# Performance work log

Measured on AMD Instinct MI355X. Metric: run time of the kernel, lower is better.

## Reference

```python
import jax, jax.numpy as jnp
import numpy as np

VOCAB = 100000
EMBED = 128

def setup_inputs() -> dict:
    key = jax.random.key(0)
    k1, k2, k3 = jax.random.split(key, 3)
    x = jax.random.randint(k1, (4096, 200), 0, VOCAB, dtype=jnp.int64)
    # torch Linear(vocab, embed): weight [embed, vocab], bias [embed]
    W = jax.random.normal(k2, (EMBED, VOCAB), dtype=jnp.float32) * (1.0 / np.sqrt(VOCAB))
    b = jax.random.normal(k3, (EMBED,), dtype=jnp.float32) * 0.01
    return {"x": x, "W": W, "b": b}

def reference(x, W, b):
    # one_hot(x) @ W.T + b  ==  gather rows of W.T at x, then add bias.
    # Same math as the original scatter+Linear, expressed as a row-gather.
    y = jnp.take(W.T, x, axis=0)  # [B, T, EMBED]
    return y + b
```

## Files before the change

### kernel.cpp

```cpp
#include <hip/hip_runtime.h>


#define EMB 128
#define TOK_PER_BLK 64

typedef float fx4 __attribute__((ext_vector_type(4)));

__global__ void transpose_W_kernel(const float* __restrict__ W,
                                   float* __restrict__ Wt, int V) {
    __shared__ float lds[64 * 129];
    const int v0 = blockIdx.x * 64;
    const int t  = threadIdx.x;

    #pragma unroll 8
    for (int j = t; j < 128 * 64; j += 256) {
        const int e    = j >> 6;
        const int vloc = j & 63;
        const int v    = v0 + vloc;
        float val = 0.0f;
        if (v < V) val = W[(size_t)e * V + v];
        lds[vloc * 129 + e] = val;
    }
    __syncthreads();

    #pragma unroll 8
    for (int j = t; j < 64 * 128; j += 256) {
        const int vloc = j >> 7;
        const int e    = j & 127;
        const int v    = v0 + vloc;
        if (v < V) Wt[(size_t)v * EMB + e] = lds[vloc * 129 + e];
    }
}

__global__ void gather_rows_kernel(const int* __restrict__ idx,
                                   const float* __restrict__ Wt,
                                   const float* __restrict__ bias,
                                   float* __restrict__ out, int ntok) {
    __shared__ int rows[TOK_PER_BLK];
    const int t    = threadIdx.x;
    const int tok0 = blockIdx.x * TOK_PER_BLK;

    if (t < TOK_PER_BLK) {
        const int tok = tok0 + t;
        rows[t] = (tok < ntok) ? idx[tok] : 0;
    }
    __syncthreads();

    const int q = t & 31;
    const int g = t >> 5;
    const fx4 bq = ((const fx4*)bias)[q];

    fx4 v[8];
    #pragma unroll
    for (int p = 0; p < 8; ++p) {
        const int row = rows[g + p * 8];
        v[p] = ((const fx4*)(Wt + (size_t)row * EMB))[q];
    }

    #pragma unroll
    for (int p = 0; p < 8; ++p) {
        const int tok = tok0 + g + p * 8;
        if (tok < ntok) {
            fx4 r = v[p] + bq;
            __builtin_nontemporal_store(r, (fx4*)(out + (size_t)tok * EMB) + q);
        }
    }
}

__global__ void gather_direct_kernel(const int* __restrict__ idx,
                                     const float* __restrict__ W,
                                     const float* __restrict__ bias,
                                     float* __restrict__ out, int ntok, int V) {
    const long long total  = (long long)ntok * EMB;
    const long long stride = (long long)gridDim.x * blockDim.x;
    for (long long i = (long long)blockIdx.x * blockDim.x + threadIdx.x;
         i < total; i += stride) {
        const int token = (int)(i >> 7);
        const int e     = (int)(i & (EMB - 1));
        out[i] = W[(size_t)e * V + idx[token]] + bias[e];
    }
}

extern "C" void kernel_launch(void* const* d_in, const int* in_sizes, int n_in,
                              void* d_out, int out_size, void* d_ws, size_t ws_size,
                              hipStream_t stream) {
    const int*   x = (const int*)d_in[0];
    const float* W = (const float*)d_in[1];
    const float* b = (const float*)d_in[2];
    float* out = (float*)d_out;

    const int ntok = in_sizes[0];
    const int V    = in_sizes[1] / EMB;

    const size_t need = (size_t)V * EMB * sizeof(float);
    if (ws_size >= need) {
        float* Wt = (float*)d_ws;
        const int tblocks = (V + 63) / 64;
        transpose_W_kernel<<<tblocks, 256, 0, stream>>>(W, Wt, V);
        const int gblocks = (ntok + TOK_PER_BLK - 1) / TOK_PER_BLK;
        gather_rows_kernel<<<gblocks, 256, 0, stream>>>(x, Wt, b, out, ntok);
    } else {
        gather_direct_kernel<<<2048, 256, 0, stream>>>(x, W, b, out, ntok, V);
    }
}
```

Baseline: 516.5 us.

## Fold bias into transposed table and use persistent grid-stride gather

Adds the bias during the W transpose, so the gathered rows already include it and the gather kernel only copies. The gather becomes a persistent kernel of 2560 blocks looping over 64-token tiles, and each thread reads its own indices straight from global memory instead of staging them in LDS behind a barrier. The aim is to remove the bias load and add, the shared-memory sync, and per-block launch overhead. In exchange the transpose does extra bias reads, and the fixed grid size may fit the CU count less well.

```diff
diff --git a/kernel.cpp b/kernel.cpp
--- a/kernel.cpp
+++ b/kernel.cpp
@@ -2,12 +2,12 @@
 
 
 #define EMB 128
-#define TOK_PER_BLK 64
 
 typedef float fx4 __attribute__((ext_vector_type(4)));
 
-__global__ void transpose_W_kernel(const float* __restrict__ W,
-                                   float* __restrict__ Wt, int V) {
+__global__ void transpose_bias_kernel(const float* __restrict__ W,
+                                      const float* __restrict__ bias,
+                                      float* __restrict__ Wt, int V) {
     __shared__ float lds[64 * 129];
     const int v0 = blockIdx.x * 64;
     const int t  = threadIdx.x;
@@ -28,41 +28,46 @@
         const int vloc = j >> 7;
         const int e    = j & 127;
         const int v    = v0 + vloc;
-        if (v < V) Wt[(size_t)v * EMB + e] = lds[vloc * 129 + e];
+        if (v < V) Wt[(size_t)v * EMB + e] = lds[vloc * 129 + e] + bias[e];
     }
 }
 
 __global__ void gather_rows_kernel(const int* __restrict__ idx,
                                    const float* __restrict__ Wt,
-                                   const float* __restrict__ bias,
                                    float* __restrict__ out, int ntok) {
-    __shared__ int rows[TOK_PER_BLK];
-    const int t    = threadIdx.x;
-    const int tok0 = blockIdx.x * TOK_PER_BLK;
-
-    if (t < TOK_PER_BLK) {
-        const int tok = tok0 + t;
-        rows[t] = (tok < ntok) ? idx[tok] : 0;
-    }
-    __syncthreads();
-
+    const int t = threadIdx.x;
     const int q = t & 31;
     const int g = t >> 5;
-    const fx4 bq = ((const fx4*)bias)[q];
+    const int ntiles = (ntok + 63) >> 6;
 
-    fx4 v[8];
-    #pragma unroll
-    for (int p = 0; p < 8; ++p) {
-        const int row = rows[g + p * 8];
-        v[p] = ((const fx4*)(Wt + (size_t)row * EMB))[q];
-    }
+    for (int tile = blockIdx.x; tile < ntiles; tile += gridDim.x) {
+        const int tok0 = tile << 6;
+        if (tok0 + 64 <= ntok) {
+            int rows[8];
+            #pragma unroll
+            for (int p = 0; p < 8; ++p)
+                rows[p] = idx[tok0 + g + (p << 3)];
 
-    #pragma unroll
-    for (int p = 0; p < 8; ++p) {
-        const int tok = tok0 + g + p * 8;
-        if (tok < ntok) {
-            fx4 r = v[p] + bq;
-            __builtin_nontemporal_store(r, (fx4*)(out + (size_t)tok * EMB) + q);
+            fx4 v[8];
+            #pragma unroll
+            for (int p = 0; p < 8; ++p)
+                v[p] = ((const fx4*)(Wt + ((size_t)rows[p] << 7)))[q];
+
+            #pragma unroll
+            for (int p = 0; p < 8; ++p)
+                __builtin_nontemporal_store(
+                    v[p], (fx4*)(out + ((size_t)(tok0 + g + (p << 3)) << 7)) + q);
+        } else {
+            #pragma unroll
+            for (int p = 0; p < 8; ++p) {
+                const int tok = tok0 + g + (p << 3);
+                if (tok < ntok) {
+                    const int row = idx[tok];
+                    fx4 v = ((const fx4*)(Wt + ((size_t)row << 7)))[q];
+                    __builtin_nontemporal_store(
+                        v, (fx4*)(out + ((size_t)tok << 7)) + q);
+                }
+            }
         }
     }
 }
@@ -96,9 +101,8 @@
     if (ws_size >= need) {
         float* Wt = (float*)d_ws;
         const int tblocks = (V + 63) / 64;
-        transpose_W_kernel<<<tblocks, 256, 0, stream>>>(W, Wt, V);
-        const int gblocks = (ntok + TOK_PER_BLK - 1) / TOK_PER_BLK;
-        gather_rows_kernel<<<gblocks, 256, 0, stream>>>(x, Wt, b, out, ntok);
+        transpose_bias_kernel<<<tblocks, 256, 0, stream>>>(W, b, Wt, V);
+        gather_rows_kernel<<<2560, 256, 0, stream>>>(x, Wt, out, ntok);
     } else {
         gather_direct_kernel<<<2048, 256, 0, stream>>>(x, W, b, out, ntok, V);
     }
```

Result: no change. 519.6 us (+0.6%).
